# Performance work log

Hardware: AMD Instinct MI355X
Metric: run time of the kernel (lower is better)

The kernel has to match this reference:

```python
import jax, jax.numpy as jnp
import numpy as np

N_NODES = 50000
N_EDGES = 800000
IN_FEATS = 128
NUM_HEADS = 4
OUT_FEATS = 32


def setup_inputs() -> dict:
    key = jax.random.key(0)
    k1, k2, k3, k4 = jax.random.split(key, 4)
    feat = jax.random.normal(k1, (N_NODES, IN_FEATS), dtype=jnp.float32)
    # nn.Linear weight: [out_features, in_features] = [H*D, in]
    W = jax.random.normal(k2, (NUM_HEADS * OUT_FEATS, IN_FEATS), dtype=jnp.float32) * (1.0 / np.sqrt(IN_FEATS))
    src = jax.random.randint(k3, (N_EDGES,), 0, N_NODES, dtype=jnp.int32)
    dst = jax.random.randint(k4, (N_EDGES,), 0, N_NODES, dtype=jnp.int32)
    return {"feat": feat, "W": W, "src": src, "dst": dst}


def reference(feat, W, src, dst):
    N = feat.shape[0]
    H, D = NUM_HEADS, OUT_FEATS
    scale = jnp.float32(1.0 / np.sqrt(D))
    # fc: feat @ W.T  ->  [N, H, D]
    ft = (feat @ W.T).reshape(N, H, D)
    ft_src = ft[src]                                   # [E, H, D] gather
    # u_dot_v: per-edge, per-head dot product, scaled by sqrt(out_feats)
    a = jnp.einsum('ehd,ehd->eh', ft_src, ft[dst]) * scale  # [E, H]
    # edge softmax normalized by destination node (numerically stable)
    m = jax.ops.segment_max(a, dst, num_segments=N)    # [N, H]
    e = jnp.exp(a - m[dst])                            # [E, H]
    s = jax.ops.segment_sum(e, dst, num_segments=N)    # [N, H]
    sa = e / s[dst]                                    # [E, H]
    # u_mul_e + sum aggregation: scatter-add weighted source features into dst
    out = jax.ops.segment_sum(ft_src * sa[:, :, None], dst, num_segments=N)  # [N, H, D]
    return out
```

## Files before the change

### kernel.cpp

```cpp
#include <hip/hip_runtime.h>
#include <math.h>

#define NN 50000
#define NE 800000
#define HH 4
#define DD 32

typedef __attribute__((ext_vector_type(8))) short short8;
typedef __attribute__((ext_vector_type(4))) float f32x4;

__device__ __forceinline__ unsigned short f2bf(float x) {
    unsigned u = __float_as_uint(x);
    unsigned r = (u + 0x7FFF + ((u >> 16) & 1)) >> 16;
    return (unsigned short)r;
}

__device__ __forceinline__ short8 pack8(float4 p, float4 q) {
    short8 r;
    r[0] = (short)f2bf(p.x); r[1] = (short)f2bf(p.y);
    r[2] = (short)f2bf(p.z); r[3] = (short)f2bf(p.w);
    r[4] = (short)f2bf(q.x); r[5] = (short)f2bf(q.y);
    r[6] = (short)f2bf(q.z); r[7] = (short)f2bf(q.w);
    return r;
}

__device__ __forceinline__ float bflo(unsigned u) { return __uint_as_float(u << 16); }
__device__ __forceinline__ float bfhi(unsigned u) { return __uint_as_float(u & 0xFFFF0000u); }

__global__ __launch_bounds__(256) void k_gemm(const float* __restrict__ feat,
                                              const float* __restrict__ W,
                                              unsigned short* __restrict__ ft, int N,
                                              const int* __restrict__ dst,
                                              int* __restrict__ cnt,
                                              int* __restrict__ pos) {
    __shared__ short8 wlds[2048];

    int tid = threadIdx.x;
#pragma unroll
    for (int j = 0; j < 8; ++j) {
        int f = tid + j * 256;
        int kc = f >> 9, ct = (f >> 6) & 7, l = f & 63;
        int o = ct * 16 + (l & 15);
        int kb = kc * 32 + ((l >> 4) << 3);
        const float* wp = W + o * 128 + kb;
        float4 p = *(const float4*)wp;
        float4 q = *(const float4*)(wp + 4);
        wlds[f] = pack8(p, q);
    }
    __syncthreads();

    int l = tid & 63;
    int w = tid >> 6;
    int row0 = blockIdx.x * 64;
    int arow = row0 + w * 16 + (l & 15);
    bool valid = arow < N;
    const float* fb = feat + (size_t)(valid ? arow : 0) * 128 + ((l >> 4) << 3);

    f32x4 acc[8];
#pragma unroll
    for (int ct = 0; ct < 8; ++ct) acc[ct] = (f32x4){0.f, 0.f, 0.f, 0.f};

#pragma unroll
    for (int kc = 0; kc < 4; ++kc) {
        short8 a;
        if (valid) {
            float4 p = *(const float4*)(fb + kc * 32);
            float4 q = *(const float4*)(fb + kc * 32 + 4);
            a = pack8(p, q);
        } else {
            a = (short8){0, 0, 0, 0, 0, 0, 0, 0};
        }
#pragma unroll
        for (int ct = 0; ct < 8; ++ct) {
            short8 b = wlds[kc * 512 + ct * 64 + l];
            acc[ct] = __builtin_amdgcn_mfma_f32_16x16x32_bf16(a, b, acc[ct], 0, 0, 0);
        }
    }

    int oc = l & 15;
    int rg = l >> 4;
#pragma unroll
    for (int i = 0; i < 4; ++i) {
        int r = row0 + w * 16 + rg * 4 + i;
        if (r < N) {
            unsigned short* op = ft + (size_t)r * 128 + oc;
#pragma unroll
            for (int ct = 0; ct < 8; ++ct) op[ct * 16] = f2bf(acc[ct][i]);
        }
    }

    int nthr = gridDim.x * 256;
    for (int e = blockIdx.x * 256 + tid; e < NE; e += nthr)
        pos[e] = atomicAdd(&cnt[dst[e]], 1);
}

__global__ __launch_bounds__(256) void k_scan1(const int* __restrict__ cnt, int* __restrict__ row,
                                               int* __restrict__ partial, int n) {
    __shared__ int sh[256];
    int i = blockIdx.x * 256 + threadIdx.x;
    int x = (i < n) ? cnt[i] : 0;
    sh[threadIdx.x] = x;
    __syncthreads();
    for (int off = 1; off < 256; off <<= 1) {
        int v = (threadIdx.x >= off) ? sh[threadIdx.x - off] : 0;
        __syncthreads();
        sh[threadIdx.x] += v;
        __syncthreads();
    }
    if (i < n) row[i] = sh[threadIdx.x] - x;
    if (threadIdx.x == 255) partial[blockIdx.x] = sh[255];
}

__global__ __launch_bounds__(256) void k_scan2(int* __restrict__ partial, int nb) {
    __shared__ int sh[256];
    int t = threadIdx.x;
    int x = (t < nb) ? partial[t] : 0;
    sh[t] = x;
    __syncthreads();
    for (int off = 1; off < 256; off <<= 1) {
        int v = (t >= off) ? sh[t - off] : 0;
        __syncthreads();
        sh[t] += v;
        __syncthreads();
    }
    if (t < nb) partial[t] = sh[t] - x;
}

__global__ __launch_bounds__(256) void k_scan3(int* __restrict__ row,
                                               const int* __restrict__ partial, int n) {
    int i = blockIdx.x * 256 + threadIdx.x;
    if (i < n) row[i] += partial[blockIdx.x];
    if (i == 0) row[n] = NE;
}

__global__ __launch_bounds__(256) void k_fill(const int* __restrict__ src, const int* __restrict__ dst,
                                              const int* __restrict__ row, const int* __restrict__ pos,
                                              int* __restrict__ srcs) {
    int e = blockIdx.x * 256 + threadIdx.x;
    if (e >= NE) return;
    srcs[row[dst[e]] + pos[e]] = src[e];
}

__global__ __launch_bounds__(256) void k_agg(const unsigned* __restrict__ ftb,
                                             const int* __restrict__ row,
                                             const int* __restrict__ srcs,
                                             float2* __restrict__ out2) {
    int n = blockIdx.x * 4 + (threadIdx.x >> 6);
    int l = threadIdx.x & 63;
    int r0 = row[n], r1 = row[n + 1];
    size_t base = (size_t)n * 64 + l;
    unsigned ud = ftb[base];
    float fdx = bflo(ud), fdy = bfhi(ud);
    float m = -INFINITY, s = 0.f;
    float ax = 0.f, ay = 0.f;
    int p = r0;
    for (; p + 1 < r1; p += 2) {
        int s0 = srcs[p], s1 = srcs[p + 1];
        unsigned u0 = ftb[(size_t)s0 * 64 + l];
        unsigned u1 = ftb[(size_t)s1 * 64 + l];
        float f0x = bflo(u0), f0y = bfhi(u0);
        float f1x = bflo(u1), f1y = bfhi(u1);
        float v0 = fdx * f0x + fdy * f0y;
        float v1 = fdx * f1x + fdy * f1y;
        v0 += __shfl_xor(v0, 1);  v1 += __shfl_xor(v1, 1);
        v0 += __shfl_xor(v0, 2);  v1 += __shfl_xor(v1, 2);
        v0 += __shfl_xor(v0, 4);  v1 += __shfl_xor(v1, 4);
        v0 += __shfl_xor(v0, 8);  v1 += __shfl_xor(v1, 8);
        v0 *= 0.17677669529663687f;
        v1 *= 0.17677669529663687f;
        float mn = fmaxf(fmaxf(m, v0), v1);
        float sc = __expf(m - mn);
        float w0 = __expf(v0 - mn);
        float w1 = __expf(v1 - mn);
        s = s * sc + w0 + w1;
        ax = ax * sc + w0 * f0x + w1 * f1x;
        ay = ay * sc + w0 * f0y + w1 * f1y;
        m = mn;
    }
    if (p < r1) {
        int s0 = srcs[p];
        unsigned u0 = ftb[(size_t)s0 * 64 + l];
        float f0x = bflo(u0), f0y = bfhi(u0);
        float v0 = fdx * f0x + fdy * f0y;
        v0 += __shfl_xor(v0, 1);
        v0 += __shfl_xor(v0, 2);
        v0 += __shfl_xor(v0, 4);
        v0 += __shfl_xor(v0, 8);
        v0 *= 0.17677669529663687f;
        float mn = fmaxf(m, v0);
        float sc = __expf(m - mn);
        float w0 = __expf(v0 - mn);
        s = s * sc + w0;
        ax = ax * sc + w0 * f0x;
        ay = ay * sc + w0 * f0y;
    }
    float inv = (r1 > r0) ? 1.f / s : 0.f;
    out2[base] = make_float2(ax * inv, ay * inv);
}

extern "C" void kernel_launch(void* const* d_in, const int* in_sizes, int n_in,
                              void* d_out, int out_size, void* d_ws, size_t ws_size,
                              hipStream_t stream) {
    const float* feat = (const float*)d_in[0];
    const float* W    = (const float*)d_in[1];
    const int*   src  = (const int*)d_in[2];
    const int*   dst  = (const int*)d_in[3];
    float* out = (float*)d_out;

    unsigned short* ft = (unsigned short*)d_ws;
    int* row  = (int*)(ft + (size_t)NN * 128);
    int* pos  = row + (NN + 1);
    int* srcs = pos + NE;
    int* cnt  = srcs + NE;
    int* part = cnt + NN;

    const int NB1 = (NN + 255) / 256;

    hipMemsetAsync(cnt, 0, (size_t)NN * sizeof(int), stream);
    k_gemm<<<(NN + 63) / 64, 256, 0, stream>>>(feat, W, ft, NN, dst, cnt, pos);
    k_scan1<<<NB1, 256, 0, stream>>>(cnt, row, part, NN);
    k_scan2<<<1, 256, 0, stream>>>(part, NB1);
    k_scan3<<<NB1, 256, 0, stream>>>(row, part, NN);
    k_fill<<<(NE + 255) / 256, 256, 0, stream>>>(src, dst, row, pos, srcs);
    k_agg<<<NN / 4, 256, 0, stream>>>((const unsigned*)ft, row, srcs, (float2*)out);
}
```

Measured before the change: 211.4 us.

## Split edge ranking out of GEMM and replace three-pass scan with single-block scan

Result: slower. 302.7 us (+43.2%).

```diff
diff --git a/kernel.cpp b/kernel.cpp
--- a/kernel.cpp
+++ b/kernel.cpp
@@ -29,10 +29,7 @@
 
 __global__ __launch_bounds__(256) void k_gemm(const float* __restrict__ feat,
                                               const float* __restrict__ W,
-                                              unsigned short* __restrict__ ft, int N,
-                                              const int* __restrict__ dst,
-                                              int* __restrict__ cnt,
-                                              int* __restrict__ pos) {
+                                              unsigned short* __restrict__ ft, int N) {
     __shared__ short8 wlds[2048];
 
     int tid = threadIdx.x;
@@ -88,49 +85,44 @@
             for (int ct = 0; ct < 8; ++ct) op[ct * 16] = f2bf(acc[ct][i]);
         }
     }
-
-    int nthr = gridDim.x * 256;
-    for (int e = blockIdx.x * 256 + tid; e < NE; e += nthr)
-        pos[e] = atomicAdd(&cnt[dst[e]], 1);
-}
-
-__global__ __launch_bounds__(256) void k_scan1(const int* __restrict__ cnt, int* __restrict__ row,
-                                               int* __restrict__ partial, int n) {
-    __shared__ int sh[256];
-    int i = blockIdx.x * 256 + threadIdx.x;
-    int x = (i < n) ? cnt[i] : 0;
-    sh[threadIdx.x] = x;
+}
+
+__global__ __launch_bounds__(256) void k_rank(const int* __restrict__ dst,
+                                              int* __restrict__ cnt,
+                                              int* __restrict__ pos) {
+    int e = blockIdx.x * 256 + threadIdx.x;
+    if (e < NE) pos[e] = atomicAdd(&cnt[dst[e]], 1);
+}
+
+__global__ __launch_bounds__(1024) void k_scan(const int* __restrict__ cnt,
+                                               int* __restrict__ row) {
+    __shared__ int sh[1024];
+    const int C = (NN + 1023) / 1024;
+    int t = threadIdx.x;
+    int i0 = t * C;
+    int sum = 0;
+    for (int j = 0; j < C; ++j) {
+        int i = i0 + j;
+        if (i < NN) sum += cnt[i];
+    }
+    sh[t] = sum;
     __syncthreads();
-    for (int off = 1; off < 256; off <<= 1) {
-        int v = (threadIdx.x >= off) ? sh[threadIdx.x - off] : 0;
-        __syncthreads();
-        sh[threadIdx.x] += v;
-        __syncthreads();
-    }
-    if (i < n) row[i] = sh[threadIdx.x] - x;
-    if (threadIdx.x == 255) partial[blockIdx.x] = sh[255];
-}
-
-__global__ __launch_bounds__(256) void k_scan2(int* __restrict__ partial, int nb) {
-    __shared__ int sh[256];
-    int t = threadIdx.x;
-    int x = (t < nb) ? partial[t] : 0;
-    sh[t] = x;
-    __syncthreads();
-    for (int off = 1; off < 256; off <<= 1) {
+    for (int off = 1; off < 1024; off <<= 1) {
         int v = (t >= off) ? sh[t - off] : 0;
         __syncthreads();
         sh[t] += v;
         __syncthreads();
     }
-    if (t < nb) partial[t] = sh[t] - x;
-}
-
-__global__ __launch_bounds__(256) void k_scan3(int* __restrict__ row,
-                                               const int* __restrict__ partial, int n) {
-    int i = blockIdx.x * 256 + threadIdx.x;
-    if (i < n) row[i] += partial[blockIdx.x];
-    if (i == 0) row[n] = NE;
+    int pre = sh[t] - sum;
+    for (int j = 0; j < C; ++j) {
+        int i = i0 + j;
+        if (i < NN) {
+            int c = cnt[i];
+            row[i] = pre;
+            pre += c;
+        }
+    }
+    if (t == 0) row[NN] = NE;
 }
 
 __global__ __launch_bounds__(256) void k_fill(const int* __restrict__ src, const int* __restrict__ dst,
@@ -212,15 +204,11 @@
     int* pos  = row + (NN + 1);
     int* srcs = pos + NE;
     int* cnt  = srcs + NE;
-    int* part = cnt + NN;
-
-    const int NB1 = (NN + 255) / 256;
 
     hipMemsetAsync(cnt, 0, (size_t)NN * sizeof(int), stream);
-    k_gemm<<<(NN + 63) / 64, 256, 0, stream>>>(feat, W, ft, NN, dst, cnt, pos);
-    k_scan1<<<NB1, 256, 0, stream>>>(cnt, row, part, NN);
-    k_scan2<<<1, 256, 0, stream>>>(part, NB1);
-    k_scan3<<<NB1, 256, 0, stream>>>(row, part, NN);
+    k_gemm<<<(NN + 63) / 64, 256, 0, stream>>>(feat, W, ft, NN);
+    k_rank<<<(NE + 255) / 256, 256, 0, stream>>>(dst, cnt, pos);
+    k_scan<<<1, 1024, 0, stream>>>(cnt, row);
     k_fill<<<(NE + 255) / 256, 256, 0, stream>>>(src, dst, row, pos, srcs);
     k_agg<<<NN / 4, 256, 0, stream>>>((const unsigned*)ft, row, srcs, (float2*)out);
 }
```
